# Optimization experiments

Measured on AMD Instinct MI355X. Metric: run time of the kernel, lower is better.

## Reference

```python
import jax, jax.numpy as jnp
import numpy as np

B, S, D, H = 2, 2048, 1024, 16
DQ = D // H
EPS = 1e-5


def setup_inputs() -> dict:
    key = jax.random.key(0)
    ks = jax.random.split(key, 6)
    scale = 0.02
    return {
        "x": jax.random.normal(ks[0], (B, S, D), dtype=jnp.float32),
        "ln_g": jnp.ones((D,), dtype=jnp.float32),
        "ln_b": jnp.zeros((D,), dtype=jnp.float32),
        "Wq": jax.random.normal(ks[1], (D, D), dtype=jnp.float32) * scale,
        "bq": jnp.zeros((D,), dtype=jnp.float32),
        "Wk": jax.random.normal(ks[2], (D, D), dtype=jnp.float32) * scale,
        "bk": jnp.zeros((D,), dtype=jnp.float32),
        "Wv": jax.random.normal(ks[3], (D, D), dtype=jnp.float32) * scale,
        "bv": jnp.zeros((D,), dtype=jnp.float32),
        "Wo": jax.random.normal(ks[4], (D, D), dtype=jnp.float32) * scale,
        "bo": jnp.zeros((D,), dtype=jnp.float32),
    }


def reference(x, ln_g, ln_b, Wq, bq, Wk, bk, Wv, bv, Wo, bo):
    # pre-LayerNorm (torch default eps=1e-5, biased variance)
    mu = jnp.mean(x, axis=-1, keepdims=True)
    var = jnp.mean((x - mu) ** 2, axis=-1, keepdims=True)
    xn = (x - mu) * jax.lax.rsqrt(var + EPS) * ln_g + ln_b

    # QKV projections; weights stored [d_in, d_out]
    q = xn @ Wq + bq  # [B,S,D]
    k = xn @ Wk + bk
    v = xn @ Wv + bv

    # split heads -> [B,H,S,DQ]
    def heads(t):
        return t.reshape(B, S, H, DQ).transpose(0, 2, 1, 3)
    q, k, v = heads(q), heads(k), heads(v)

    scores = jnp.einsum("bhqd,bhkd->bhqk", q, k) / jnp.sqrt(jnp.float32(DQ))
    causal = jnp.tril(jnp.ones((S, S), dtype=bool))  # True = keep
    scores = jnp.where(causal, scores, -jnp.inf)
    probs = jax.nn.softmax(scores, axis=-1)
    attn = jnp.einsum("bhqk,bhkd->bhqd", probs, v)  # [B,H,S,DQ]

    # merge heads: [B,H,S,DQ] -> [B,S,H*DQ] (matches transpose/flatten/transpose)
    merged = attn.transpose(0, 2, 1, 3).reshape(B, S, D)
    out = merged @ Wo + bo
    return out + x
```

## Files before the change

### kernel.cpp

```cpp
#include <hip/hip_runtime.h>
#include <math.h>

#define BB 2
#define SS 2048
#define DD 1024
#define HH 16
#define DQK 64
#define NROWS (BB * SS)
#define NE ((size_t)BB * SS * DD)

using short8 = __attribute__((ext_vector_type(8))) short;
using f32x4  = __attribute__((ext_vector_type(4))) float;

__device__ __forceinline__ ushort f2bf(float f) {
  union { float f; unsigned u; } c; c.f = f;
  return (ushort)((c.u + 0x7fffu + ((c.u >> 16) & 1u)) >> 16);
}

__device__ __forceinline__ unsigned cvt_pk_bf16(float lo, float hi) {
  unsigned r;
  asm("v_cvt_pk_bf16_f32 %0, %1, %2" : "=v"(r) : "v"(lo), "v"(hi));
  return r;
}

__device__ __forceinline__ f32x4 mfma16(short8 a, short8 b, f32x4 c) {
  return __builtin_amdgcn_mfma_f32_16x16x32_bf16(a, b, c, 0, 0, 0);
}

typedef __attribute__((address_space(1))) const unsigned gas_u32;
typedef __attribute__((address_space(3))) unsigned las_u32;
__device__ __forceinline__ void gload_lds16(const void* g, void* l) {
  __builtin_amdgcn_global_load_lds((gas_u32*)g, (las_u32*)l, 16, 0, 0);
}

__global__ __launch_bounds__(256) void ln_fwd(const float* __restrict__ x,
                                              const float* __restrict__ g,
                                              const float* __restrict__ bta,
                                              ushort* __restrict__ xn) {
  const int row = blockIdx.x;
  const int t = threadIdx.x;
  float4 v = ((const float4*)(x + (size_t)row * DD))[t];
  float s  = v.x + v.y + v.z + v.w;
  float ss = v.x * v.x + v.y * v.y + v.z * v.z + v.w * v.w;
#pragma unroll
  for (int off = 32; off > 0; off >>= 1) {
    s  += __shfl_xor(s, off);
    ss += __shfl_xor(ss, off);
  }
  __shared__ float red[8];
  const int wid = t >> 6, lane = t & 63;
  if (lane == 0) { red[wid] = s; red[4 + wid] = ss; }
  __syncthreads();
  const float stot  = red[0] + red[1] + red[2] + red[3];
  const float sstot = red[4] + red[5] + red[6] + red[7];
  const float mu  = stot * (1.0f / DD);
  const float var = sstot * (1.0f / DD) - mu * mu;
  const float inv = rsqrtf(var + 1e-5f);
  const float4 g4 = ((const float4*)g)[t];
  const float4 b4 = ((const float4*)bta)[t];
  ushort4 o;
  o.x = f2bf((v.x - mu) * inv * g4.x + b4.x);
  o.y = f2bf((v.y - mu) * inv * g4.y + b4.y);
  o.z = f2bf((v.z - mu) * inv * g4.z + b4.z);
  o.w = f2bf((v.w - mu) * inv * g4.w + b4.w);
  ((ushort4*)(xn + (size_t)row * DD))[t] = o;
}

__global__ __launch_bounds__(256) void wtrans(const float* __restrict__ Wq,
                                              const float* __restrict__ Wk,
                                              const float* __restrict__ Wv,
                                              const float* __restrict__ Wo,
                                              ushort* __restrict__ wt) {
  const int z = blockIdx.z;
  const float* W = (z == 0) ? Wq : (z == 1) ? Wk : (z == 2) ? Wv : Wo;
  ushort* dst = wt + (size_t)z * DD * DD;
  __shared__ float tile[64][65];
  const int t = threadIdx.x;
  const int k0 = blockIdx.x * 64, n0 = blockIdx.y * 64;
  const int tr = t >> 4, tc = (t & 15) * 4;
#pragma unroll
  for (int rr = 0; rr < 64; rr += 16) {
    float4 v = *(const float4*)(W + (size_t)(k0 + rr + tr) * DD + n0 + tc);
    tile[rr + tr][tc + 0] = v.x;
    tile[rr + tr][tc + 1] = v.y;
    tile[rr + tr][tc + 2] = v.z;
    tile[rr + tr][tc + 3] = v.w;
  }
  __syncthreads();
#pragma unroll
  for (int rr = 0; rr < 64; rr += 16) {
    const int n = rr + tr;
    ushort4 o;
    o.x = f2bf(tile[tc + 0][n]);
    o.y = f2bf(tile[tc + 1][n]);
    o.z = f2bf(tile[tc + 2][n]);
    o.w = f2bf(tile[tc + 3][n]);
    *(ushort4*)(dst + (size_t)(n0 + n) * DD + k0 + tc) = o;
  }
}

#define GEMM_CORE(Ag, Bg)                                                     \
  f32x4 acc[4][4];                                                            \
  _Pragma("unroll")                                                           \
  for (int m = 0; m < 4; ++m)                                                 \
    _Pragma("unroll")                                                         \
    for (int n = 0; n < 4; ++n) acc[m][n] = (f32x4){0.f, 0.f, 0.f, 0.f};     \
  const int cs = ((t & 3) * 16) ^ (((t >> 2) & 3) * 16);                      \
  const int fsw = (r16 & 3) * 16;                                             \
  {                                                                           \
    GSTAGE(Ag, Bg, 0, 0);                                                     \
    int cur = 0;                                                              \
    for (int k0 = 0; k0 < DD; k0 += 32) {                                     \
      asm volatile("s_waitcnt vmcnt(0)" ::: "memory");                        \
      __syncthreads();                                                        \
      if (k0 + 32 < DD) GSTAGE(Ag, Bg, cur ^ 1, k0 + 32);                     \
      const char* Ac = (const char*)&As[cur][0][0];                           \
      const char* Bc = (const char*)&Bs[cur][0][0];                           \
      short8 af[4], bf[4];                                                    \
      _Pragma("unroll")                                                       \
      for (int m = 0; m < 4; ++m)                                             \
        af[m] = *(const short8*)(Ac + (wr * 64 + m * 16 + r16) * 64 +         \
                                 ((g * 16) ^ fsw));                           \
      _Pragma("unroll")                                                       \
      for (int n = 0; n < 4; ++n)                                             \
        bf[n] = *(const short8*)(Bc + (wc * 64 + n * 16 + r16) * 64 +         \
                                 ((g * 16) ^ fsw));                           \
      _Pragma("unroll")                                                       \
      for (int m = 0; m < 4; ++m)                                             \
        _Pragma("unroll")                                                     \
        for (int n = 0; n < 4; ++n) acc[m][n] = mfma16(af[m], bf[n], acc[m][n]); \
      cur ^= 1;                                                               \
    }                                                                         \
  }

#define GSTAGE(Ag, Bg, buf, k0)                                               \
  {                                                                           \
    _Pragma("unroll")                                                         \
    for (int i = 0; i < 2; ++i) {                                             \
      gload_lds16(Ag + (size_t)(row0 + i * 64 + (t >> 2)) * (DD * 2) +        \
                      (k0) * 2 + cs,                                          \
                  (char*)&As[buf][0][0] + i * 4096 + t * 16);                 \
      gload_lds16(Bg + (size_t)(col0 + i * 64 + (t >> 2)) * (DD * 2) +        \
                      (k0) * 2 + cs,                                          \
                  (char*)&Bs[buf][0][0] + i * 4096 + t * 16);                 \
    }                                                                         \
  }

__global__ __launch_bounds__(256) void gemm_qkv(
    const ushort* __restrict__ A, const ushort* __restrict__ wt,
    const float* __restrict__ bq, const float* __restrict__ bk,
    const float* __restrict__ bv, ushort* __restrict__ qb,
    ushort* __restrict__ kb, ushort* __restrict__ vt) {
  __shared__ ushort As[2][128][32];
  __shared__ ushort Bs[2][128][32];
  const int t = threadIdx.x;
  const int lane = t & 63;
  const int w = t >> 6, wr = w >> 1, wc = w & 1;
  const int r16 = lane & 15, g = lane >> 4;
  const int row0 = blockIdx.x * 128;
  const int mat = blockIdx.y >> 3;
  const int col0 = (blockIdx.y & 7) * 128;
  const char* Ag = (const char*)A;
  const char* Bg = (const char*)(wt + (size_t)mat * DD * DD);
  const float* bias = (mat == 0) ? bq : (mat == 1) ? bk : bv;

  GEMM_CORE(Ag, Bg)

#pragma unroll
  for (int n = 0; n < 4; ++n) {
    const int c = col0 + wc * 64 + n * 16 + r16;
    const float bc = bias[c];
#pragma unroll
    for (int m = 0; m < 4; ++m) {
      const int rbase = row0 + wr * 64 + m * 16 + g * 4;
      if (mat < 2) {
        ushort* outb = (mat == 0) ? qb : kb;
#pragma unroll
        for (int e = 0; e < 4; ++e)
          outb[(size_t)(rbase + e) * DD + c] = f2bf(acc[m][n][e] + bc);
      } else {
        uint2 st;
        st.x = cvt_pk_bf16(acc[m][n][0] + bc, acc[m][n][1] + bc);
        st.y = cvt_pk_bf16(acc[m][n][2] + bc, acc[m][n][3] + bc);
        const size_t vrow = (size_t)((rbase >> 11) * HH + (c >> 6)) * DQK + (c & 63);
        *(uint2*)(vt + vrow * SS + (rbase & 2047)) = st;
      }
    }
  }
}

__global__ __launch_bounds__(256) void gemm_o(
    const ushort* __restrict__ A, const ushort* __restrict__ Bt,
    const float* __restrict__ bias, const float* __restrict__ resid,
    float* __restrict__ outf) {
  __shared__ ushort As[2][128][32];
  __shared__ ushort Bs[2][128][32];
  const int t = threadIdx.x;
  const int lane = t & 63;
  const int w = t >> 6, wr = w >> 1, wc = w & 1;
  const int r16 = lane & 15, g = lane >> 4;
  const int row0 = blockIdx.x * 128;
  const int col0 = blockIdx.y * 128;
  const char* Ag = (const char*)A;
  const char* Bg = (const char*)Bt;

  GEMM_CORE(Ag, Bg)

#pragma unroll
  for (int n = 0; n < 4; ++n) {
    const int c = col0 + wc * 64 + n * 16 + r16;
    const float bc = bias[c];
#pragma unroll
    for (int m = 0; m < 4; ++m) {
      const int rbase = row0 + wr * 64 + m * 16 + g * 4;
#pragma unroll
      for (int e = 0; e < 4; ++e) {
        const size_t idx = (size_t)(rbase + e) * DD + c;
        outf[idx] = acc[m][n][e] + bc + resid[idx];
      }
    }
  }
}

__global__ __launch_bounds__(256) void attn_mfma(const ushort* __restrict__ Q,
                                                 const ushort* __restrict__ K,
                                                 const ushort* __restrict__ Vt,
                                                 ushort* __restrict__ O) {
  __shared__ ushort Ks[2][64][64];
  __shared__ ushort Vs[2][64][64];
  __shared__ ushort Ps[4][16][64];

  const int t = threadIdx.x, lane = t & 63, ww = t >> 6;
  const int r16 = lane & 15, g = lane >> 4;

  const int bid = blockIdx.x;
  const int xcd = bid & 7, idx = bid >> 3;
  const int bh = xcd * 4 + (idx & 3);
  const int pp = idx >> 2;
  const int b = bh >> 4, h = bh & 15;
  const size_t tokbase = (size_t)b * SS;
  const size_t hoff = (size_t)h * DQK;

  const int srow = t >> 3;
  const int scol = (t & 7) * 16;
  const char* Kb = (const char*)(K + tokbase * DD + hoff);
  const char* Vb = (const char*)(Vt + (size_t)bh * DQK * SS);
  const int sw = (r16 & 7) << 4;
  const float SCL = 0.125f * 1.44269504f;

#define STAGE(buf, j0)                                                        \
  {                                                                           \
    _Pragma("unroll")                                                         \
    for (int i = 0; i < 2; ++i) {                                             \
      const int R = i * 32 + srow;                                            \
      const int Cs = scol ^ ((R & 7) << 4);                                   \
      gload_lds16(Kb + ((size_t)((j0) + R) * DD) * 2 + Cs,                    \
                  (char*)&Ks[buf][0][0] + i * 4096 + ww * 1024);              \
      gload_lds16(Vb + ((size_t)R * SS + (j0)) * 2 + Cs,                      \
                  (char*)&Vs[buf][0][0] + i * 4096 + ww * 1024);              \
    }                                                                         \
  }

  for (int seg = 0; seg < 2; ++seg) {
    const int qb = seg ? (31 - pp) : pp;
    const int q0 = qb * 64 + ww * 16;
    const int nt = qb + 1;

    short8 qf[2];
#pragma unroll
    for (int kc = 0; kc < 2; ++kc)
      qf[kc] = *(const short8*)(Q + (tokbase + q0 + r16) * DD + hoff + kc * 32 + g * 8);

    f32x4 o[4];
#pragma unroll
    for (int dt = 0; dt < 4; ++dt) o[dt] = (f32x4){0.f, 0.f, 0.f, 0.f};
    float rm = -INFINITY, rl = 0.f;
    const int thr = q0 + r16 - g * 4;

    __syncthreads();
    STAGE(0, 0);
    int cur = 0;
    for (int tt = 0; tt < nt; ++tt) {
      asm volatile("s_waitcnt vmcnt(0)" ::: "memory");
      __syncthreads();
      if (tt + 1 < nt) STAGE(cur ^ 1, (tt + 1) * 64);

      const char* Kc = (const char*)&Ks[cur][0][0];
      const char* Vc = (const char*)&Vs[cur][0][0];

      f32x4 s4[4];
      __builtin_amdgcn_s_setprio(1);
#pragma unroll
      for (int t2 = 0; t2 < 4; ++t2) {
        const int rb = (t2 * 16 + r16) * 128;
        const short8 k0 = *(const short8*)(Kc + rb + ((g * 16) ^ sw));
        const short8 k1 = *(const short8*)(Kc + rb + ((64 + g * 16) ^ sw));
        f32x4 s = mfma16(k0, qf[0], (f32x4){0.f, 0.f, 0.f, 0.f});
        s4[t2] = mfma16(k1, qf[1], s);
      }
      __builtin_amdgcn_s_setprio(0);

      float sv[4][4];
      const bool last = (tt == nt - 1);
#pragma unroll
      for (int t2 = 0; t2 < 4; ++t2)
#pragma unroll
        for (int r = 0; r < 4; ++r) {
          float xv = s4[t2][r] * SCL;
          if (last) xv = (tt * 64 + t2 * 16 + r <= thr) ? xv : -INFINITY;
          sv[t2][r] = xv;
        }

      float mx = fmaxf(fmaxf(fmaxf(sv[0][0], sv[0][1]), fmaxf(sv[0][2], sv[0][3])),
                       fmaxf(fmaxf(sv[1][0], sv[1][1]), fmaxf(sv[1][2], sv[1][3])));
      mx = fmaxf(mx, fmaxf(fmaxf(fmaxf(sv[2][0], sv[2][1]), fmaxf(sv[2][2], sv[2][3])),
                           fmaxf(fmaxf(sv[3][0], sv[3][1]), fmaxf(sv[3][2], sv[3][3]))));
      mx = fmaxf(mx, __shfl_xor(mx, 16));
      mx = fmaxf(mx, __shfl_xor(mx, 32));
      if (!__all(mx - rm <= 8.f)) {
        const float mn = fmaxf(rm, mx);
        const float sc = __builtin_amdgcn_exp2f(rm - mn);
        rl *= sc;
#pragma unroll
        for (int dt = 0; dt < 4; ++dt) o[dt] *= sc;
        rm = mn;
      }
      float ps = 0.f;
#pragma unroll
      for (int t2 = 0; t2 < 4; ++t2) {
        const float p0 = __builtin_amdgcn_exp2f(sv[t2][0] - rm);
        const float p1 = __builtin_amdgcn_exp2f(sv[t2][1] - rm);
        const float p2 = __builtin_amdgcn_exp2f(sv[t2][2] - rm);
        const float p3 = __builtin_amdgcn_exp2f(sv[t2][3] - rm);
        ps += (p0 + p1) + (p2 + p3);
        uint2 pk;
        pk.x = cvt_pk_bf16(p0, p1);
        pk.y = cvt_pk_bf16(p2, p3);
        *(uint2*)((char*)&Ps[ww][0][0] + r16 * 128 + ((t2 * 32 + g * 8) ^ sw)) = pk;
      }
      ps += __shfl_xor(ps, 16);
      ps += __shfl_xor(ps, 32);
      rl += ps;

      __builtin_amdgcn_s_setprio(1);
#pragma unroll
      for (int kc = 0; kc < 2; ++kc) {
        const short8 pb = *(const short8*)((const char*)&Ps[ww][0][0] + r16 * 128 +
                                           ((kc * 64 + g * 16) ^ sw));
#pragma unroll
        for (int dt = 0; dt < 4; ++dt) {
          const short8 vf = *(const short8*)(Vc + (dt * 16 + r16) * 128 +
                                             ((kc * 64 + g * 16) ^ sw));
          o[dt] = mfma16(vf, pb, o[dt]);
        }
      }
      __builtin_amdgcn_s_setprio(0);
      cur ^= 1;
    }

    const float inv = 1.0f / rl;
#pragma unroll
    for (int dt = 0; dt < 4; ++dt) {
      uint2 st;
      st.x = cvt_pk_bf16(o[dt][0] * inv, o[dt][1] * inv);
      st.y = cvt_pk_bf16(o[dt][2] * inv, o[dt][3] * inv);
      *(uint2*)(O + (tokbase + q0 + r16) * DD + hoff + dt * 16 + g * 4) = st;
    }
  }
#undef STAGE
}

extern "C" void kernel_launch(void* const* d_in, const int* in_sizes, int n_in,
                              void* d_out, int out_size, void* d_ws, size_t ws_size,
                              hipStream_t stream) {
  const float* x    = (const float*)d_in[0];
  const float* ln_g = (const float*)d_in[1];
  const float* ln_b = (const float*)d_in[2];
  const float* Wq   = (const float*)d_in[3];
  const float* bq   = (const float*)d_in[4];
  const float* Wk   = (const float*)d_in[5];
  const float* bk   = (const float*)d_in[6];
  const float* Wv   = (const float*)d_in[7];
  const float* bv   = (const float*)d_in[8];
  const float* Wo   = (const float*)d_in[9];
  const float* bo   = (const float*)d_in[10];
  float* out = (float*)d_out;

  ushort* ws  = (ushort*)d_ws;
  ushort* xn  = ws;
  ushort* qb  = xn + NE;
  ushort* kb  = qb + NE;
  ushort* vt  = kb + NE;
  ushort* ab  = vt + NE;
  ushort* wt  = ab + NE;
  ushort* wot = wt + (size_t)3 * DD * DD;

  wtrans<<<dim3(16, 16, 4), 256, 0, stream>>>(Wq, Wk, Wv, Wo, wt);
  ln_fwd<<<NROWS, 256, 0, stream>>>(x, ln_g, ln_b, xn);

  gemm_qkv<<<dim3(NROWS / 128, 24), 256, 0, stream>>>(xn, wt, bq, bk, bv,
                                                      qb, kb, vt);

  attn_mfma<<<BB * HH * (SS / 128), 256, 0, stream>>>(qb, kb, vt, ab);

  gemm_o<<<dim3(NROWS / 128, DD / 128), 256, 0, stream>>>(ab, wot, bo, x, out);
}
```

Baseline: 121.2 us.

## Split attention into one q-block per workgroup and fold softmax scale into Q

The attention grid is doubled so each workgroup handles a single 64-row query block, launched longest-first, instead of pairing short and long blocks in one workgroup. The softmax scale is folded into the Q projection epilogue, removing a multiply per score. Cross-lane reductions for the row max now run only when a rescale is triggered, and the row sum is reduced once after the loop. Tail imbalance now relies on hardware scheduling rather than explicit pairing.

```diff
diff --git a/kernel.cpp b/kernel.cpp
--- a/kernel.cpp
+++ b/kernel.cpp
@@ -163,6 +163,7 @@
   const char* Ag = (const char*)A;
   const char* Bg = (const char*)(wt + (size_t)mat * DD * DD);
   const float* bias = (mat == 0) ? bq : (mat == 1) ? bk : bv;
+  const float scl = (mat == 0) ? 0.125f * 1.44269504f : 1.0f;
 
   GEMM_CORE(Ag, Bg)
 
@@ -177,7 +178,7 @@
         ushort* outb = (mat == 0) ? qb : kb;
 #pragma unroll
         for (int e = 0; e < 4; ++e)
-          outb[(size_t)(rbase + e) * DD + c] = f2bf(acc[m][n][e] + bc);
+          outb[(size_t)(rbase + e) * DD + c] = f2bf((acc[m][n][e] + bc) * scl);
       } else {
         uint2 st;
         st.x = cvt_pk_bf16(acc[m][n][0] + bc, acc[m][n][1] + bc);
@@ -236,17 +237,18 @@
   const int bid = blockIdx.x;
   const int xcd = bid & 7, idx = bid >> 3;
   const int bh = xcd * 4 + (idx & 3);
-  const int pp = idx >> 2;
+  const int qb = 31 - (idx >> 2);
   const int b = bh >> 4, h = bh & 15;
   const size_t tokbase = (size_t)b * SS;
   const size_t hoff = (size_t)h * DQK;
+  const int q0 = qb * 64 + ww * 16;
+  const int nt = qb + 1;
 
   const int srow = t >> 3;
   const int scol = (t & 7) * 16;
   const char* Kb = (const char*)(K + tokbase * DD + hoff);
   const char* Vb = (const char*)(Vt + (size_t)bh * DQK * SS);
   const int sw = (r16 & 7) << 4;
-  const float SCL = 0.125f * 1.44269504f;
 
 #define STAGE(buf, j0)                                                        \
   {                                                                           \
@@ -261,113 +263,104 @@
     }                                                                         \
   }
 
-  for (int seg = 0; seg < 2; ++seg) {
-    const int qb = seg ? (31 - pp) : pp;
-    const int q0 = qb * 64 + ww * 16;
-    const int nt = qb + 1;
-
-    short8 qf[2];
-#pragma unroll
-    for (int kc = 0; kc < 2; ++kc)
-      qf[kc] = *(const short8*)(Q + (tokbase + q0 + r16) * DD + hoff + kc * 32 + g * 8);
-
-    f32x4 o[4];
-#pragma unroll
-    for (int dt = 0; dt < 4; ++dt) o[dt] = (f32x4){0.f, 0.f, 0.f, 0.f};
-    float rm = -INFINITY, rl = 0.f;
-    const int thr = q0 + r16 - g * 4;
-
+  short8 qf[2];
+#pragma unroll
+  for (int kc = 0; kc < 2; ++kc)
+    qf[kc] = *(const short8*)(Q + (tokbase + q0 + r16) * DD + hoff + kc * 32 + g * 8);
+
+  f32x4 o[4];
+#pragma unroll
+  for (int dt = 0; dt < 4; ++dt) o[dt] = (f32x4){0.f, 0.f, 0.f, 0.f};
+  float rm = -INFINITY, rl = 0.f;
+  const int thr = q0 + r16 - g * 4;
+
+  STAGE(0, 0);
+  int cur = 0;
+  for (int tt = 0; tt < nt; ++tt) {
+    asm volatile("s_waitcnt vmcnt(0)" ::: "memory");
     __syncthreads();
-    STAGE(0, 0);
-    int cur = 0;
-    for (int tt = 0; tt < nt; ++tt) {
-      asm volatile("s_waitcnt vmcnt(0)" ::: "memory");
-      __syncthreads();
-      if (tt + 1 < nt) STAGE(cur ^ 1, (tt + 1) * 64);
-
-      const char* Kc = (const char*)&Ks[cur][0][0];
-      const char* Vc = (const char*)&Vs[cur][0][0];
-
-      f32x4 s4[4];
-      __builtin_amdgcn_s_setprio(1);
-#pragma unroll
-      for (int t2 = 0; t2 < 4; ++t2) {
-        const int rb = (t2 * 16 + r16) * 128;
-        const short8 k0 = *(const short8*)(Kc + rb + ((g * 16) ^ sw));
-        const short8 k1 = *(const short8*)(Kc + rb + ((64 + g * 16) ^ sw));
-        f32x4 s = mfma16(k0, qf[0], (f32x4){0.f, 0.f, 0.f, 0.f});
-        s4[t2] = mfma16(k1, qf[1], s);
+    if (tt + 1 < nt) STAGE(cur ^ 1, (tt + 1) * 64);
+
+    const char* Kc = (const char*)&Ks[cur][0][0];
+    const char* Vc = (const char*)&Vs[cur][0][0];
+
+    f32x4 s4[4];
+    __builtin_amdgcn_s_setprio(1);
+#pragma unroll
+    for (int t2 = 0; t2 < 4; ++t2) {
+      const int rb = (t2 * 16 + r16) * 128;
+      const short8 k0 = *(const short8*)(Kc + rb + ((g * 16) ^ sw));
+      const short8 k1 = *(const short8*)(Kc + rb + ((64 + g * 16) ^ sw));
+      f32x4 s = mfma16(k0, qf[0], (f32x4){0.f, 0.f, 0.f, 0.f});
+      s4[t2] = mfma16(k1, qf[1], s);
+    }
+    __builtin_amdgcn_s_setprio(0);
+
+    if (tt == nt - 1) {
+#pragma unroll
+      for (int t2 = 0; t2 < 4; ++t2)
+#pragma unroll
+        for (int r = 0; r < 4; ++r)
+          s4[t2][r] = (tt * 64 + t2 * 16 + r <= thr) ? s4[t2][r] : -INFINITY;
+    }
+
+    float mx = fmaxf(
+        fmaxf(fmaxf(fmaxf(s4[0][0], s4[0][1]), fmaxf(s4[0][2], s4[0][3])),
+              fmaxf(fmaxf(s4[1][0], s4[1][1]), fmaxf(s4[1][2], s4[1][3]))),
+        fmaxf(fmaxf(fmaxf(s4[2][0], s4[2][1]), fmaxf(s4[2][2], s4[2][3])),
+              fmaxf(fmaxf(s4[3][0], s4[3][1]), fmaxf(s4[3][2], s4[3][3]))));
+
+    if (!__all(mx - rm <= 8.f)) {
+      float mf = fmaxf(mx, __shfl_xor(mx, 16));
+      mf = fmaxf(mf, __shfl_xor(mf, 32));
+      const float mn = fmaxf(rm, mf);
+      const float sc = __builtin_amdgcn_exp2f(rm - mn);
+      rl *= sc;
+#pragma unroll
+      for (int dt = 0; dt < 4; ++dt) o[dt] *= sc;
+      rm = mn;
+    }
+
+#pragma unroll
+    for (int t2 = 0; t2 < 4; ++t2) {
+      const float p0 = __builtin_amdgcn_exp2f(s4[t2][0] - rm);
+      const float p1 = __builtin_amdgcn_exp2f(s4[t2][1] - rm);
+      const float p2 = __builtin_amdgcn_exp2f(s4[t2][2] - rm);
+      const float p3 = __builtin_amdgcn_exp2f(s4[t2][3] - rm);
+      rl += (p0 + p1) + (p2 + p3);
+      uint2 pk;
+      pk.x = cvt_pk_bf16(p0, p1);
+      pk.y = cvt_pk_bf16(p2, p3);
+      *(uint2*)((char*)&Ps[ww][0][0] + r16 * 128 + ((t2 * 32 + g * 8) ^ sw)) = pk;
+    }
+
+    __builtin_amdgcn_s_setprio(1);
+#pragma unroll
+    for (int kc = 0; kc < 2; ++kc) {
+      const short8 pb = *(const short8*)((const char*)&Ps[ww][0][0] + r16 * 128 +
+                                         ((kc * 64 + g * 16) ^ sw));
+#pragma unroll
+      for (int dt = 0; dt < 4; ++dt) {
+        const short8 vf = *(const short8*)(Vc + (dt * 16 + r16) * 128 +
+                                           ((kc * 64 + g * 16) ^ sw));
+        o[dt] = mfma16(vf, pb, o[dt]);
       }
-      __builtin_amdgcn_s_setprio(0);
-
-      float sv[4][4];
-      const bool last = (tt == nt - 1);
-#pragma unroll
-      for (int t2 = 0; t2 < 4; ++t2)
-#pragma unroll
-        for (int r = 0; r < 4; ++r) {
-          float xv = s4[t2][r] * SCL;
-          if (last) xv = (tt * 64 + t2 * 16 + r <= thr) ? xv : -INFINITY;
-          sv[t2][r] = xv;
-        }
-
-      float mx = fmaxf(fmaxf(fmaxf(sv[0][0], sv[0][1]), fmaxf(sv[0][2], sv[0][3])),
-                       fmaxf(fmaxf(sv[1][0], sv[1][1]), fmaxf(sv[1][2], sv[1][3])));
-      mx = fmaxf(mx, fmaxf(fmaxf(fmaxf(sv[2][0], sv[2][1]), fmaxf(sv[2][2], sv[2][3])),
-                           fmaxf(fmaxf(sv[3][0], sv[3][1]), fmaxf(sv[3][2], sv[3][3]))));
-      mx = fmaxf(mx, __shfl_xor(mx, 16));
-      mx = fmaxf(mx, __shfl_xor(mx, 32));
-      if (!__all(mx - rm <= 8.f)) {
-        const float mn = fmaxf(rm, mx);
-        const float sc = __builtin_amdgcn_exp2f(rm - mn);
-        rl *= sc;
-#pragma unroll
-        for (int dt = 0; dt < 4; ++dt) o[dt] *= sc;
-        rm = mn;
-      }
-      float ps = 0.f;
-#pragma unroll
-      for (int t2 = 0; t2 < 4; ++t2) {
-        const float p0 = __builtin_amdgcn_exp2f(sv[t2][0] - rm);
-        const float p1 = __builtin_amdgcn_exp2f(sv[t2][1] - rm);
-        const float p2 = __builtin_amdgcn_exp2f(sv[t2][2] - rm);
-        const float p3 = __builtin_amdgcn_exp2f(sv[t2][3] - rm);
-        ps += (p0 + p1) + (p2 + p3);
-        uint2 pk;
-        pk.x = cvt_pk_bf16(p0, p1);
-        pk.y = cvt_pk_bf16(p2, p3);
-        *(uint2*)((char*)&Ps[ww][0][0] + r16 * 128 + ((t2 * 32 + g * 8) ^ sw)) = pk;
-      }
-      ps += __shfl_xor(ps, 16);
-      ps += __shfl_xor(ps, 32);
-      rl += ps;
-
-      __builtin_amdgcn_s_setprio(1);
-#pragma unroll
-      for (int kc = 0; kc < 2; ++kc) {
-        const short8 pb = *(const short8*)((const char*)&Ps[ww][0][0] + r16 * 128 +
-                                           ((kc * 64 + g * 16) ^ sw));
-#pragma unroll
-        for (int dt = 0; dt < 4; ++dt) {
-          const short8 vf = *(const short8*)(Vc + (dt * 16 + r16) * 128 +
-                                             ((kc * 64 + g * 16) ^ sw));
-          o[dt] = mfma16(vf, pb, o[dt]);
-        }
-      }
-      __builtin_amdgcn_s_setprio(0);
-      cur ^= 1;
-    }
-
-    const float inv = 1.0f / rl;
-#pragma unroll
-    for (int dt = 0; dt < 4; ++dt) {
-      uint2 st;
-      st.x = cvt_pk_bf16(o[dt][0] * inv, o[dt][1] * inv);
-      st.y = cvt_pk_bf16(o[dt][2] * inv, o[dt][3] * inv);
-      *(uint2*)(O + (tokbase + q0 + r16) * DD + hoff + dt * 16 + g * 4) = st;
-    }
+    }
+    __builtin_amdgcn_s_setprio(0);
+    cur ^= 1;
   }
 #undef STAGE
+
+  rl += __shfl_xor(rl, 16);
+  rl += __shfl_xor(rl, 32);
+  const float inv = 1.0f / rl;
+#pragma unroll
+  for (int dt = 0; dt < 4; ++dt) {
+    uint2 st;
+    st.x = cvt_pk_bf16(o[dt][0] * inv, o[dt][1] * inv);
+    st.y = cvt_pk_bf16(o[dt][2] * inv, o[dt][3] * inv);
+    *(uint2*)(O + (tokbase + q0 + r16) * DD + hoff + dt * 16 + g * 4) = st;
+  }
 }
 
 extern "C" void kernel_launch(void* const* d_in, const int* in_sizes, int n_in,
@@ -401,7 +394,7 @@
   gemm_qkv<<<dim3(NROWS / 128, 24), 256, 0, stream>>>(xn, wt, bq, bk, bv,
                                                       qb, kb, vt);
 
-  attn_mfma<<<BB * HH * (SS / 128), 256, 0, stream>>>(qb, kb, vt, ab);
+  attn_mfma<<<BB * HH * (SS / 64), 256, 0, stream>>>(qb, kb, vt, ab);
 
   gemm_o<<<dim3(NROWS / 128, DD / 128), 256, 0, stream>>>(ab, wot, bo, x, out);
 }
```

Result: faster. 118.8 us (-2.0%).
